# Kernel tuning notes

Hardware: AMD Instinct MI355X
Metric: run time of the kernel (lower is better)

## Reference

```python
import jax, jax.numpy as jnp
import numpy as np

B, S, H = 4, 512, 1024
E, K, I = 8, 2, 2048

def setup_inputs() -> dict:
    key = jax.random.key(0)
    k1, k2, k3, k4, k5 = jax.random.split(key, 5)
    scale_h = 1.0 / np.sqrt(H)
    scale_i = 1.0 / np.sqrt(I)
    return {
        "hidden_states": jax.random.normal(k1, (B, S, H), dtype=jnp.float32),
        "router_w": jax.random.normal(k2, (E, H), dtype=jnp.float32) * scale_h,
        "w_gate": jax.random.normal(k3, (E, H, I), dtype=jnp.float32) * scale_h,
        "w_up": jax.random.normal(k4, (E, H, I), dtype=jnp.float32) * scale_h,
        "w_down": jax.random.normal(k5, (E, I, H), dtype=jnp.float32) * scale_i,
    }

def reference(hidden_states, router_w, w_gate, w_up, w_down):
    b, s, h = hidden_states.shape
    x = hidden_states.reshape(-1, h)              # [T, H] tokens
    T = x.shape[0]

    # ---- RouterTopK: fp32 linear -> softmax over all experts -> top-k ----
    router_logits = x.astype(jnp.float32) @ router_w.T          # [T, E]
    probs = jax.nn.softmax(router_logits, axis=-1)               # [T, E]
    top_vals, top_idx = jax.lax.top_k(probs, K)                  # [T, K]

    # normalize_top_k_affinities (norm_topk_prob=True)
    top_vals = top_vals / jnp.sum(top_vals, axis=-1, keepdims=True)

    # scatter normalized affinities into a dense [T, E] combine matrix
    aff = jnp.zeros((T, E), dtype=x.dtype).at[jnp.arange(T)[:, None], top_idx].set(top_vals.astype(x.dtype))

    # ---- ExpertMLPs: GLU (swiglu) per expert, combine weighted by affinity ----
    # Dense-per-expert computation; non-selected experts contribute 0 via aff.
    gate = jnp.einsum('th,ehi->eti', x, w_gate)                  # [E, T, I]
    up = jnp.einsum('th,ehi->eti', x, w_up)                      # [E, T, I]
    act = jax.nn.silu(gate) * up                                 # [E, T, I]
    expert_out = jnp.einsum('eti,eih->eth', act, w_down)         # [E, T, H]
    out = jnp.einsum('eth,te->th', expert_out, aff)              # [T, H]

    # _reduce_output: all-reduce over TP/world group -> identity single-device
    return out.reshape(b, s, h)
```

## Files before the change

kernel.cpp:

```cpp
#include <hip/hip_runtime.h>
#include <hip/hip_bf16.h>

#define T_TOK 2048
#define H_DIM 1024
#define E_N   8
#define I_DIM 2048

#define NT_MAX 40
#define MAX_SLOTS 5120

typedef unsigned short u16;
typedef unsigned int   u32;
typedef __bf16 bf16_t;
typedef bf16_t bf16x8 __attribute__((ext_vector_type(8)));
typedef u16    u16x8  __attribute__((ext_vector_type(8)));
typedef float  f32x4  __attribute__((ext_vector_type(4)));

#define MFMA __builtin_amdgcn_mfma_f32_16x16x32_bf16

__device__ __forceinline__ u16 bfbits(float f) {
    bf16_t b = (bf16_t)f;
    return __builtin_bit_cast(u16, b);
}

__device__ __forceinline__ void gload_lds16(const void* g, void* l) {
    __builtin_amdgcn_global_load_lds(
        (const __attribute__((address_space(1))) void*)g,
        (__attribute__((address_space(3))) void*)l, 16, 0, 0);
}

__device__ __forceinline__ int tile_off(int n, int kb) {
    return n * 64 + ((kb ^ ((n >> 1) & 7)) << 3);
}
__device__ __forceinline__ int a_off(int row, int kslot) {
    return row * 64 + ((kslot ^ (row & 7)) << 3);
}

__global__ __launch_bounds__(256) void router_k(
    const float* __restrict__ x, const float* __restrict__ rw,
    int* __restrict__ cnt, int* __restrict__ tok, float* __restrict__ wts,
    u16* __restrict__ xbf)
{
    int wid = threadIdx.x >> 6, lane = threadIdx.x & 63;
    int t = blockIdx.x * 4 + wid;
    const float* xr = x + (size_t)t * H_DIM;
    u16* xbr = xbf + (size_t)t * H_DIM;

    float acc[E_N];
#pragma unroll
    for (int e = 0; e < E_N; e++) acc[e] = 0.f;
    for (int j = 0; j < H_DIM / 64; j++) {
        float xv = xr[lane + 64 * j];
        xbr[lane + 64 * j] = bfbits(xv);
#pragma unroll
        for (int e = 0; e < E_N; e++)
            acc[e] += xv * rw[e * H_DIM + lane + 64 * j];
    }
#pragma unroll
    for (int e = 0; e < E_N; e++) {
        float v = acc[e];
        for (int off = 32; off; off >>= 1) v += __shfl_xor(v, off);
        acc[e] = v;
    }
    if (lane == 0) {
        int i0 = 0; float m0 = acc[0];
#pragma unroll
        for (int e = 1; e < E_N; e++) if (acc[e] > m0) { m0 = acc[e]; i0 = e; }
        int i1 = -1; float m1 = -INFINITY;
#pragma unroll
        for (int e = 0; e < E_N; e++) if (e != i0 && acc[e] > m1) { m1 = acc[e]; i1 = e; }
        float w0 = 1.f / (1.f + expf(m1 - m0));
        float w1 = 1.f - w0;
        int p0 = atomicAdd(&cnt[i0], 1);
        tok[i0 * T_TOK + p0] = t; wts[i0 * T_TOK + p0] = w0;
        int p1 = atomicAdd(&cnt[i1], 1);
        tok[i1 * T_TOK + p1] = t; wts[i1 * T_TOK + p1] = w1;
    }
}

__global__ void prefix_k(const int* __restrict__ cnt, int* __restrict__ offs_pad,
                         int* __restrict__ tile_e, int* __restrict__ tile_row0,
                         int* __restrict__ ntiles)
{
    if (threadIdx.x == 0) {
        int s = 0, nt = 0;
        for (int e = 0; e < E_N; e++) {
            offs_pad[e] = s;
            int c = cnt[e];
            int t = (c + 127) >> 7;
            for (int i = 0; i < t; i++) { tile_e[nt] = e; tile_row0[nt] = i * 128; nt++; }
            s += t * 128;
        }
        offs_pad[E_N] = s;
        *ntiles = nt;
    }
}

__global__ __launch_bounds__(512, 2) void gateup_k(
    const u16* __restrict__ xbf, const float* __restrict__ wg, const float* __restrict__ wu,
    const int* __restrict__ cnt, const int* __restrict__ offs_pad,
    const int* __restrict__ tile_e, const int* __restrict__ tile_row0,
    const int* __restrict__ ntiles, const int* __restrict__ tok,
    u16* __restrict__ act)
{
    int q = gridDim.x >> 3;
    int phys = blockIdx.x;
    int logical = (phys & 7) * q + (phys >> 3);
    int tb = logical % NT_MAX;
    int p  = logical / NT_MAX;
    if (tb >= *ntiles) return;
    int e = tile_e[tb], row0 = tile_row0[tb];
    int cntE = cnt[e];
    int slot0 = offs_pad[e] + row0;
    int n0 = p * 128;

    __shared__ u16 AS[2][8192], GS[2][8192], US[2][8192];

    int tid = threadIdx.x;
    int lane = tid & 63, wid = tid >> 6;
    int wm = wid & 3, wn = wid >> 2;
    int l15 = lane & 15, lg = lane >> 4;

    const u16* asrc[2];
#pragma unroll
    for (int i = 0; i < 2; i++) {
        int row = (wid * 2 + i) * 8 + (lane >> 3);
        int rc = (row0 + row < cntE) ? (row0 + row) : (cntE - 1);
        asrc[i] = xbf + (size_t)tok[e * T_TOK + rc] * H_DIM + (((lane & 7) ^ (lane >> 3)) << 3);
    }
    int s0 = (wid * 2) * 512;

    int mat   = tid >> 8;
    int tid8  = tid & 255;
    int bn    = tid8 & 127;
    int khalf = tid8 >> 7;
    const float* wsrc = (mat ? wu : wg)
        + ((size_t)e * H_DIM + khalf * 32) * I_DIM + n0 + bn;

    float v[32];

#define B_LOAD(t) { \
    _Pragma("unroll") \
    for (int j = 0; j < 32; j++) \
        v[j] = wsrc[(size_t)((t) * 64 + j) * I_DIM]; }

#define B_WRITE(nbuf) { \
    u16* bdst = mat ? US[nbuf] : GS[nbuf]; \
    _Pragma("unroll") \
    for (int jb = 0; jb < 4; jb++) { \
        u16x8 pk; \
        _Pragma("unroll") \
        for (int jj = 0; jj < 8; jj++) pk[jj] = bfbits(v[jb * 8 + jj]); \
        *reinterpret_cast<u16x8*>(&bdst[tile_off(bn, khalf * 4 + jb)]) = pk; \
    } }

#define A_STAGE(nbuf, t) { \
    gload_lds16(asrc[0] + (size_t)(t) * 64, &AS[nbuf][s0]); \
    gload_lds16(asrc[1] + (size_t)(t) * 64, &AS[nbuf][s0 + 512]); }

    f32x4 accg[2][4], accu[2][4];
#pragma unroll
    for (int a = 0; a < 2; a++)
#pragma unroll
        for (int b = 0; b < 4; b++) { accg[a][b] = (f32x4)0.f; accu[a][b] = (f32x4)0.f; }

    A_STAGE(0, 0);
    B_LOAD(0);
    B_WRITE(0);
    __syncthreads();

#pragma unroll 2
    for (int t = 0; t < 16; t++) {
        int buf = t & 1;
        bool more = (t + 1) < 16;
        if (more) {
            A_STAGE(buf ^ 1, t + 1);
            B_LOAD(t + 1);
        }
        __builtin_amdgcn_sched_barrier(0);

#pragma unroll
        for (int ks = 0; ks < 2; ks++) {
            bf16x8 af[2];
#pragma unroll
            for (int mf = 0; mf < 2; mf++) {
                int row = wm * 32 + mf * 16 + l15;
                af[mf] = *reinterpret_cast<const bf16x8*>(&AS[buf][a_off(row, ks * 4 + lg)]);
            }
            int kbr = ks * 4 + lg;
#pragma unroll
            for (int nf = 0; nf < 4; nf++) {
                int c = wn * 64 + nf * 16 + l15;
                int o = tile_off(c, kbr);
                bf16x8 bg = *reinterpret_cast<const bf16x8*>(&GS[buf][o]);
                bf16x8 bu = *reinterpret_cast<const bf16x8*>(&US[buf][o]);
#pragma unroll
                for (int mf = 0; mf < 2; mf++) {
                    accg[mf][nf] = MFMA(af[mf], bg, accg[mf][nf], 0, 0, 0);
                    accu[mf][nf] = MFMA(af[mf], bu, accu[mf][nf], 0, 0, 0);
                }
            }
        }

        if (more) B_WRITE(buf ^ 1);
        __syncthreads();
    }
#undef B_LOAD
#undef B_WRITE
#undef A_STAGE

#pragma unroll
    for (int mf = 0; mf < 2; mf++)
#pragma unroll
        for (int j = 0; j < 4; j++) {
            int rl = wm * 32 + mf * 16 + lg * 4 + j;
            bool valid = (row0 + rl) < cntE;
            size_t base = (size_t)(slot0 + rl) * I_DIM + n0;
#pragma unroll
            for (int nf = 0; nf < 4; nf++) {
                float g = accg[mf][nf][j];
                float u = accu[mf][nf][j];
                float a = valid ? (g / (1.f + expf(-g))) * u : 0.f;
                act[base + wn * 64 + nf * 16 + l15] = bfbits(a);
            }
        }
}

__global__ __launch_bounds__(512, 4) void down_k(
    const u16* __restrict__ act, const float* __restrict__ wd,
    const int* __restrict__ cnt, const int* __restrict__ offs_pad,
    const int* __restrict__ tile_e, const int* __restrict__ tile_row0,
    const int* __restrict__ ntiles, const int* __restrict__ tok,
    const float* __restrict__ wts, float* __restrict__ out)
{
    int q = gridDim.x >> 3;
    int phys = blockIdx.x;
    int logical = (phys & 7) * q + (phys >> 3);
    int tb = logical % NT_MAX;
    int rest = logical / NT_MAX;
    int p  = rest & 7;
    int kh = rest >> 3;
    if (tb >= *ntiles) return;
    int e = tile_e[tb], row0 = tile_row0[tb];
    int cntE = cnt[e];
    int slot0 = offs_pad[e] + row0;
    int h0 = p * 128;

    __shared__ u16 AS[2][8192], DS[2][8192];

    int tid = threadIdx.x;
    int lane = tid & 63, wid = tid >> 6;
    int wm = wid & 3, wn = wid >> 2;
    int l15 = lane & 15, lg = lane >> 4;

    const u16* asrc[2];
#pragma unroll
    for (int i = 0; i < 2; i++) {
        int row = (wid * 2 + i) * 8 + (lane >> 3);
        asrc[i] = act + (size_t)(slot0 + row) * I_DIM + kh * 1024
                  + (((lane & 7) ^ (lane >> 3)) << 3);
    }
    int s0 = (wid * 2) * 512;

    int bn = tid & 127;
    int kq = tid >> 7;
    const float* dsrc = wd + ((size_t)e * I_DIM + kh * 1024 + kq * 16) * H_DIM + h0 + bn;

    float v[16];

#define B_LOAD(t) { \
    _Pragma("unroll") \
    for (int j = 0; j < 16; j++) \
        v[j] = dsrc[(size_t)((t) * 64 + j) * H_DIM]; }

#define B_WRITE(nbuf) { \
    _Pragma("unroll") \
    for (int jb = 0; jb < 2; jb++) { \
        u16x8 pk; \
        _Pragma("unroll") \
        for (int jj = 0; jj < 8; jj++) pk[jj] = bfbits(v[jb * 8 + jj]); \
        *reinterpret_cast<u16x8*>(&DS[nbuf][tile_off(bn, kq * 2 + jb)]) = pk; \
    } }

#define A_STAGE(nbuf, t) { \
    gload_lds16(asrc[0] + (size_t)(t) * 64, &AS[nbuf][s0]); \
    gload_lds16(asrc[1] + (size_t)(t) * 64, &AS[nbuf][s0 + 512]); }

    f32x4 acc[2][4];
#pragma unroll
    for (int a = 0; a < 2; a++)
#pragma unroll
        for (int b = 0; b < 4; b++) acc[a][b] = (f32x4)0.f;

    A_STAGE(0, 0);
    B_LOAD(0);
    B_WRITE(0);
    __syncthreads();

#pragma unroll 2
    for (int t = 0; t < 16; t++) {
        int buf = t & 1;
        bool more = (t + 1) < 16;
        if (more) {
            A_STAGE(buf ^ 1, t + 1);
            B_LOAD(t + 1);
        }
        __builtin_amdgcn_sched_barrier(0);

#pragma unroll
        for (int ks = 0; ks < 2; ks++) {
            bf16x8 af[2];
#pragma unroll
            for (int mf = 0; mf < 2; mf++) {
                int row = wm * 32 + mf * 16 + l15;
                af[mf] = *reinterpret_cast<const bf16x8*>(&AS[buf][a_off(row, ks * 4 + lg)]);
            }
            int kbr = ks * 4 + lg;
#pragma unroll
            for (int nf = 0; nf < 4; nf++) {
                int c = wn * 64 + nf * 16 + l15;
                bf16x8 bd = *reinterpret_cast<const bf16x8*>(&DS[buf][tile_off(c, kbr)]);
#pragma unroll
                for (int mf = 0; mf < 2; mf++)
                    acc[mf][nf] = MFMA(af[mf], bd, acc[mf][nf], 0, 0, 0);
            }
        }

        if (more) B_WRITE(buf ^ 1);
        __syncthreads();
    }
#undef B_LOAD
#undef B_WRITE
#undef A_STAGE

#pragma unroll
    for (int mf = 0; mf < 2; mf++)
#pragma unroll
        for (int j = 0; j < 4; j++) {
            int rl = wm * 32 + mf * 16 + lg * 4 + j;
            int gr = row0 + rl;
            if (gr < cntE) {
                float w = wts[e * T_TOK + gr];
                int t   = tok[e * T_TOK + gr];
                size_t base = (size_t)t * H_DIM + h0;
#pragma unroll
                for (int nf = 0; nf < 4; nf++)
                    atomicAdd(&out[base + wn * 64 + nf * 16 + l15], acc[mf][nf][j] * w);
            }
        }
}

extern "C" void kernel_launch(void* const* d_in, const int* in_sizes, int n_in,
                              void* d_out, int out_size, void* d_ws, size_t ws_size,
                              hipStream_t stream)
{
    const float* x  = (const float*)d_in[0];
    const float* rw = (const float*)d_in[1];
    const float* wg = (const float*)d_in[2];
    const float* wu = (const float*)d_in[3];
    const float* wd = (const float*)d_in[4];
    float* out = (float*)d_out;

    char* ws = (char*)d_ws;
    int*   cnt       = (int*)(ws);
    int*   ntiles    = (int*)(ws + 32);
    int*   offs_pad  = (int*)(ws + 64);
    int*   tile_e    = (int*)(ws + 256);
    int*   tile_row0 = (int*)(ws + 512);
    int*   tok       = (int*)(ws + 64 * 1024);
    float* wts       = (float*)(ws + 128 * 1024);
    u16*   xbf       = (u16*)(ws + 256 * 1024);
    u16*   act       = (u16*)(ws + 4608 * 1024);

    size_t need = 4608ull * 1024 + (size_t)MAX_SLOTS * I_DIM * 2;
    if (ws_size < need) return;

    hipMemsetAsync(cnt, 0, 32, stream);
    hipMemsetAsync(out, 0, (size_t)T_TOK * H_DIM * sizeof(float), stream);

    router_k<<<T_TOK / 4, 256, 0, stream>>>(x, rw, cnt, tok, wts, xbf);
    prefix_k<<<1, 64, 0, stream>>>(cnt, offs_pad, tile_e, tile_row0, ntiles);
    gateup_k<<<NT_MAX * (I_DIM / 128), 512, 0, stream>>>(
        xbf, wg, wu, cnt, offs_pad, tile_e, tile_row0, ntiles, tok, act);
    down_k<<<NT_MAX * (H_DIM / 128) * 2, 512, 0, stream>>>(
        act, wd, cnt, offs_pad, tile_e, tile_row0, ntiles, tok, wts, out);
}
```

Before: 218.1 us.

## Prefetch weight tiles two steps ahead with explicit waitcnt pipelining in MoE GEMMs

Both the gate/up and down expert GEMMs move from a single register staging buffer to two alternating register sets. Weight loads now go out two k-steps ahead, and a manually unrolled loop uses explicit s_waitcnt vmcnt counts, raw s_barrier and sched_barrier fences in place of __syncthreads. The gate/up kernel also changes its load split so every thread loads both the gate and the up weights over a quarter of K, instead of one matrix over half of K. The aim is to hide global fp32 weight load latency behind MFMA work, at the cost of more registers and fragile hand-tuned wait counts.

Measured after the change: 218.8 us. No clear change (+0.3%).

```diff
diff --git a/kernel.cpp b/kernel.cpp
--- a/kernel.cpp
+++ b/kernel.cpp
@@ -128,33 +128,31 @@
         int rc = (row0 + row < cntE) ? (row0 + row) : (cntE - 1);
         asrc[i] = xbf + (size_t)tok[e * T_TOK + rc] * H_DIM + (((lane & 7) ^ (lane >> 3)) << 3);
     }
-    int s0 = (wid * 2) * 512;
-
-    int mat   = tid >> 8;
-    int tid8  = tid & 255;
-    int bn    = tid8 & 127;
-    int khalf = tid8 >> 7;
-    const float* wsrc = (mat ? wu : wg)
-        + ((size_t)e * H_DIM + khalf * 32) * I_DIM + n0 + bn;
-
-    float v[32];
-
-#define B_LOAD(t) { \
-    _Pragma("unroll") \
-    for (int j = 0; j < 32; j++) \
-        v[j] = wsrc[(size_t)((t) * 64 + j) * I_DIM]; }
-
-#define B_WRITE(nbuf) { \
-    u16* bdst = mat ? US[nbuf] : GS[nbuf]; \
-    _Pragma("unroll") \
-    for (int jb = 0; jb < 4; jb++) { \
-        u16x8 pk; \
-        _Pragma("unroll") \
-        for (int jj = 0; jj < 8; jj++) pk[jj] = bfbits(v[jb * 8 + jj]); \
-        *reinterpret_cast<u16x8*>(&bdst[tile_off(bn, khalf * 4 + jb)]) = pk; \
-    } }
-
-#define A_STAGE(nbuf, t) { \
+    int s0 = wid * 1024;
+
+    int bn = tid & 127;
+    int kq = tid >> 7;
+    const float* gsrc = wg + (size_t)e * H_DIM * I_DIM + n0 + bn;
+    const float* usrc = wu + (size_t)e * H_DIM * I_DIM + n0 + bn;
+
+    float g0[16], u0[16], g1[16], u1[16];
+
+#define BLOAD(gs, us, t) { \
+    _Pragma("unroll") \
+    for (int j = 0; j < 16; j++) { \
+        gs[j] = gsrc[(size_t)((t) * 64 + kq * 16 + j) * I_DIM]; \
+        us[j] = usrc[(size_t)((t) * 64 + kq * 16 + j) * I_DIM]; } }
+
+#define BWRITE(gs, us, nbuf) { \
+    _Pragma("unroll") \
+    for (int jb = 0; jb < 2; jb++) { \
+        u16x8 pg, pu; \
+        _Pragma("unroll") \
+        for (int jj = 0; jj < 8; jj++) { pg[jj] = bfbits(gs[jb * 8 + jj]); pu[jj] = bfbits(us[jb * 8 + jj]); } \
+        *reinterpret_cast<u16x8*>(&GS[nbuf][tile_off(bn, kq * 2 + jb)]) = pg; \
+        *reinterpret_cast<u16x8*>(&US[nbuf][tile_off(bn, kq * 2 + jb)]) = pu; } }
+
+#define ASTAGE(nbuf, t) { \
     gload_lds16(asrc[0] + (size_t)(t) * 64, &AS[nbuf][s0]); \
     gload_lds16(asrc[1] + (size_t)(t) * 64, &AS[nbuf][s0 + 512]); }
 
@@ -164,50 +162,78 @@
 #pragma unroll
         for (int b = 0; b < 4; b++) { accg[a][b] = (f32x4)0.f; accu[a][b] = (f32x4)0.f; }
 
-    A_STAGE(0, 0);
-    B_LOAD(0);
-    B_WRITE(0);
-    __syncthreads();
-
-#pragma unroll 2
-    for (int t = 0; t < 16; t++) {
-        int buf = t & 1;
-        bool more = (t + 1) < 16;
-        if (more) {
-            A_STAGE(buf ^ 1, t + 1);
-            B_LOAD(t + 1);
-        }
-        __builtin_amdgcn_sched_barrier(0);
-
-#pragma unroll
-        for (int ks = 0; ks < 2; ks++) {
-            bf16x8 af[2];
-#pragma unroll
-            for (int mf = 0; mf < 2; mf++) {
-                int row = wm * 32 + mf * 16 + l15;
-                af[mf] = *reinterpret_cast<const bf16x8*>(&AS[buf][a_off(row, ks * 4 + lg)]);
+#define CLUSTER(bufi) { \
+    _Pragma("unroll") \
+    for (int ks = 0; ks < 2; ks++) { \
+        bf16x8 af[2]; \
+        _Pragma("unroll") \
+        for (int mf = 0; mf < 2; mf++) { \
+            int row = wm * 32 + mf * 16 + l15; \
+            af[mf] = *reinterpret_cast<const bf16x8*>(&AS[bufi][a_off(row, ks * 4 + lg)]); } \
+        int kbr = ks * 4 + lg; \
+        _Pragma("unroll") \
+        for (int nf = 0; nf < 4; nf++) { \
+            int c = wn * 64 + nf * 16 + l15; \
+            int o = tile_off(c, kbr); \
+            bf16x8 bg = *reinterpret_cast<const bf16x8*>(&GS[bufi][o]); \
+            bf16x8 bu = *reinterpret_cast<const bf16x8*>(&US[bufi][o]); \
+            _Pragma("unroll") \
+            for (int mf = 0; mf < 2; mf++) { \
+                accg[mf][nf] = MFMA(af[mf], bg, accg[mf][nf], 0, 0, 0); \
+                accu[mf][nf] = MFMA(af[mf], bu, accu[mf][nf], 0, 0, 0); } } } }
+
+    ASTAGE(0, 0);
+    __builtin_amdgcn_sched_barrier(0);
+    BLOAD(g0, u0, 0);
+    __builtin_amdgcn_sched_barrier(0);
+    BLOAD(g1, u1, 1);
+    __builtin_amdgcn_sched_barrier(0);
+    BWRITE(g0, u0, 0);
+    __builtin_amdgcn_sched_barrier(0);
+    asm volatile("s_waitcnt vmcnt(0) lgkmcnt(0)" ::: "memory");
+    __builtin_amdgcn_s_barrier();
+    __builtin_amdgcn_sched_barrier(0);
+
+    for (int t2 = 0; t2 < 16; t2 += 2) {
+        if (t2 + 1 < 16) ASTAGE(1, t2 + 1);
+        CLUSTER(0);
+        __builtin_amdgcn_sched_barrier(0);
+        if (t2 + 1 < 16) BWRITE(g1, u1, 1);
+        __builtin_amdgcn_sched_barrier(0);
+        if (t2 + 2 < 16) {
+            BLOAD(g0, u0, t2 + 2);
+            __builtin_amdgcn_sched_barrier(0);
+            asm volatile("s_waitcnt vmcnt(32) lgkmcnt(0)" ::: "memory");
+        } else {
+            asm volatile("s_waitcnt vmcnt(0) lgkmcnt(0)" ::: "memory");
+        }
+        __builtin_amdgcn_s_barrier();
+        __builtin_amdgcn_sched_barrier(0);
+
+        {
+            int t = t2 + 1;
+            if (t + 1 < 16) ASTAGE(0, t + 1);
+            CLUSTER(1);
+            __builtin_amdgcn_sched_barrier(0);
+            if (t + 1 < 16) {
+                BWRITE(g0, u0, 0);
+                __builtin_amdgcn_sched_barrier(0);
+                if (t + 2 < 16) {
+                    BLOAD(g1, u1, t + 2);
+                    __builtin_amdgcn_sched_barrier(0);
+                    asm volatile("s_waitcnt vmcnt(32) lgkmcnt(0)" ::: "memory");
+                } else {
+                    asm volatile("s_waitcnt vmcnt(0) lgkmcnt(0)" ::: "memory");
+                }
+                __builtin_amdgcn_s_barrier();
+                __builtin_amdgcn_sched_barrier(0);
             }
-            int kbr = ks * 4 + lg;
-#pragma unroll
-            for (int nf = 0; nf < 4; nf++) {
-                int c = wn * 64 + nf * 16 + l15;
-                int o = tile_off(c, kbr);
-                bf16x8 bg = *reinterpret_cast<const bf16x8*>(&GS[buf][o]);
-                bf16x8 bu = *reinterpret_cast<const bf16x8*>(&US[buf][o]);
-#pragma unroll
-                for (int mf = 0; mf < 2; mf++) {
-                    accg[mf][nf] = MFMA(af[mf], bg, accg[mf][nf], 0, 0, 0);
-                    accu[mf][nf] = MFMA(af[mf], bu, accu[mf][nf], 0, 0, 0);
-                }
-            }
-        }
-
-        if (more) B_WRITE(buf ^ 1);
-        __syncthreads();
-    }
-#undef B_LOAD
-#undef B_WRITE
-#undef A_STAGE
+        }
+    }
+#undef BLOAD
+#undef BWRITE
+#undef ASTAGE
+#undef CLUSTER
 
 #pragma unroll
     for (int mf = 0; mf < 2; mf++)
@@ -260,29 +286,28 @@
         asrc[i] = act + (size_t)(slot0 + row) * I_DIM + kh * 1024
                   + (((lane & 7) ^ (lane >> 3)) << 3);
     }
-    int s0 = (wid * 2) * 512;
+    int s0 = wid * 1024;
 
     int bn = tid & 127;
     int kq = tid >> 7;
-    const float* dsrc = wd + ((size_t)e * I_DIM + kh * 1024 + kq * 16) * H_DIM + h0 + bn;
-
-    float v[16];
-
-#define B_LOAD(t) { \
+    const float* dsrc = wd + ((size_t)e * I_DIM + kh * 1024) * H_DIM + h0 + bn;
+
+    float v0[16], v1[16];
+
+#define BLOAD(vs, t) { \
     _Pragma("unroll") \
     for (int j = 0; j < 16; j++) \
-        v[j] = dsrc[(size_t)((t) * 64 + j) * H_DIM]; }
-
-#define B_WRITE(nbuf) { \
+        vs[j] = dsrc[(size_t)((t) * 64 + kq * 16 + j) * H_DIM]; }
+
+#define BWRITE(vs, nbuf) { \
     _Pragma("unroll") \
     for (int jb = 0; jb < 2; jb++) { \
         u16x8 pk; \
         _Pragma("unroll") \
-        for (int jj = 0; jj < 8; jj++) pk[jj] = bfbits(v[jb * 8 + jj]); \
-        *reinterpret_cast<u16x8*>(&DS[nbuf][tile_off(bn, kq * 2 + jb)]) = pk; \
-    } }
-
-#define A_STAGE(nbuf, t) { \
+        for (int jj = 0; jj < 8; jj++) pk[jj] = bfbits(vs[jb * 8 + jj]); \
+        *reinterpret_cast<u16x8*>(&DS[nbuf][tile_off(bn, kq * 2 + jb)]) = pk; } }
+
+#define ASTAGE(nbuf, t) { \
     gload_lds16(asrc[0] + (size_t)(t) * 64, &AS[nbuf][s0]); \
     gload_lds16(asrc[1] + (size_t)(t) * 64, &AS[nbuf][s0 + 512]); }
 
@@ -292,46 +317,75 @@
 #pragma unroll
         for (int b = 0; b < 4; b++) acc[a][b] = (f32x4)0.f;
 
-    A_STAGE(0, 0);
-    B_LOAD(0);
-    B_WRITE(0);
-    __syncthreads();
-
-#pragma unroll 2
-    for (int t = 0; t < 16; t++) {
-        int buf = t & 1;
-        bool more = (t + 1) < 16;
-        if (more) {
-            A_STAGE(buf ^ 1, t + 1);
-            B_LOAD(t + 1);
-        }
-        __builtin_amdgcn_sched_barrier(0);
-
-#pragma unroll
-        for (int ks = 0; ks < 2; ks++) {
-            bf16x8 af[2];
-#pragma unroll
-            for (int mf = 0; mf < 2; mf++) {
-                int row = wm * 32 + mf * 16 + l15;
-                af[mf] = *reinterpret_cast<const bf16x8*>(&AS[buf][a_off(row, ks * 4 + lg)]);
+#define CLUSTER(bufi) { \
+    _Pragma("unroll") \
+    for (int ks = 0; ks < 2; ks++) { \
+        bf16x8 af[2]; \
+        _Pragma("unroll") \
+        for (int mf = 0; mf < 2; mf++) { \
+            int row = wm * 32 + mf * 16 + l15; \
+            af[mf] = *reinterpret_cast<const bf16x8*>(&AS[bufi][a_off(row, ks * 4 + lg)]); } \
+        int kbr = ks * 4 + lg; \
+        _Pragma("unroll") \
+        for (int nf = 0; nf < 4; nf++) { \
+            int c = wn * 64 + nf * 16 + l15; \
+            bf16x8 bd = *reinterpret_cast<const bf16x8*>(&DS[bufi][tile_off(c, kbr)]); \
+            _Pragma("unroll") \
+            for (int mf = 0; mf < 2; mf++) \
+                acc[mf][nf] = MFMA(af[mf], bd, acc[mf][nf], 0, 0, 0); } } }
+
+    ASTAGE(0, 0);
+    __builtin_amdgcn_sched_barrier(0);
+    BLOAD(v0, 0);
+    __builtin_amdgcn_sched_barrier(0);
+    BLOAD(v1, 1);
+    __builtin_amdgcn_sched_barrier(0);
+    BWRITE(v0, 0);
+    __builtin_amdgcn_sched_barrier(0);
+    asm volatile("s_waitcnt vmcnt(0) lgkmcnt(0)" ::: "memory");
+    __builtin_amdgcn_s_barrier();
+    __builtin_amdgcn_sched_barrier(0);
+
+    for (int t2 = 0; t2 < 16; t2 += 2) {
+        if (t2 + 1 < 16) ASTAGE(1, t2 + 1);
+        CLUSTER(0);
+        __builtin_amdgcn_sched_barrier(0);
+        if (t2 + 1 < 16) BWRITE(v1, 1);
+        __builtin_amdgcn_sched_barrier(0);
+        if (t2 + 2 < 16) {
+            BLOAD(v0, t2 + 2);
+            __builtin_amdgcn_sched_barrier(0);
+            asm volatile("s_waitcnt vmcnt(16) lgkmcnt(0)" ::: "memory");
+        } else {
+            asm volatile("s_waitcnt vmcnt(0) lgkmcnt(0)" ::: "memory");
+        }
+        __builtin_amdgcn_s_barrier();
+        __builtin_amdgcn_sched_barrier(0);
+
+        {
+            int t = t2 + 1;
+            if (t + 1 < 16) ASTAGE(0, t + 1);
+            CLUSTER(1);
+            __builtin_amdgcn_sched_barrier(0);
+            if (t + 1 < 16) {
+                BWRITE(v0, 0);
+                __builtin_amdgcn_sched_barrier(0);
+                if (t + 2 < 16) {
+                    BLOAD(v1, t + 2);
+                    __builtin_amdgcn_sched_barrier(0);
+                    asm volatile("s_waitcnt vmcnt(16) lgkmcnt(0)" ::: "memory");
+                } else {
+                    asm volatile("s_waitcnt vmcnt(0) lgkmcnt(0)" ::: "memory");
+                }
+                __builtin_amdgcn_s_barrier();
+                __builtin_amdgcn_sched_barrier(0);
             }
-            int kbr = ks * 4 + lg;
-#pragma unroll
-            for (int nf = 0; nf < 4; nf++) {
-                int c = wn * 64 + nf * 16 + l15;
-                bf16x8 bd = *reinterpret_cast<const bf16x8*>(&DS[buf][tile_off(c, kbr)]);
-#pragma unroll
-                for (int mf = 0; mf < 2; mf++)
-                    acc[mf][nf] = MFMA(af[mf], bd, acc[mf][nf], 0, 0, 0);
-            }
-        }
-
-        if (more) B_WRITE(buf ^ 1);
-        __syncthreads();
-    }
-#undef B_LOAD
-#undef B_WRITE
-#undef A_STAGE
+        }
+    }
+#undef BLOAD
+#undef BWRITE
+#undef ASTAGE
+#undef CLUSTER
 
 #pragma unroll
     for (int mf = 0; mf < 2; mf++)
```
